# Performance work log

Measured on AMD Instinct MI355X. Metric: run time of the kernel, lower is better.

The kernel has to match this reference:

```python
import jax, jax.numpy as jnp
import numpy as np

MINUS = -100.0
PIECE_NUM = 3

def setup_inputs() -> dict:
    key = jax.random.key(0)
    kx, km = jax.random.split(key)
    B, C, L = 256, 768, 256
    x = jax.random.normal(kx, (B, C, L), dtype=jnp.float32)
    # piece ids in 0..piece_num (0 = padding -> zero row of identity embedding)
    mask = jax.random.randint(km, (B, L), 0, PIECE_NUM + 1, dtype=jnp.int64)
    return {"x": x, "mask": mask}

def reference(x, mask):
    # x: (B, C, L); mask: (B, L) ints in [0, piece_num]
    B, C, L = x.shape
    # mask_embedding weight = [zeros(1,P); I(P)], so emb(mask)[b,l,p] = (mask[b,l] == p+1)
    onehot = (mask[:, :, None] == jnp.arange(1, PIECE_NUM + 1)).astype(x.dtype)  # (B, L, P)
    # mask_embedded = 1 - emb(mask).transpose(1,2).unsqueeze(2): (B, P, 1, L)
    bias = MINUS * (1.0 - onehot.transpose(0, 2, 1))[:, :, None, :]  # (B, P, 1, L)
    # x.unsqueeze(1) + minus * mask_embedded -> (B, P, C, L); max-pool over L
    pooled = jnp.max(x[:, None, :, :] + bias, axis=-1)  # (B, P, C)
    return pooled.reshape(B, PIECE_NUM * C)  # piece-major, matches view([B, -1])
```

## Files before the change

### kernel.cpp

```cpp
#include <hip/hip_runtime.h>


constexpr int BB = 256;
constexpr int CC = 768;
constexpr int LL = 256;
constexpr int PP = 3;
constexpr float MINUS = -100.0f;

constexpr int ROWS_PER_WAVE  = 12;
constexpr int WAVES_PER_BLOCK = 4;
constexpr int ROWS_PER_BLOCK = ROWS_PER_WAVE * WAVES_PER_BLOCK;
constexpr int BLOCKS_PER_B   = CC / ROWS_PER_BLOCK;

__global__ __launch_bounds__(256) void piece_max_pool_kernel(
    const float* __restrict__ x,
    const int*   __restrict__ mask,
    float*       __restrict__ out)
{
    const int tid  = threadIdx.x;
    const int lane = tid & 63;
    const int wave = tid >> 6;
    const int blk  = blockIdx.x;
    const int b    = blk / BLOCKS_PER_B;
    const int cbase = (blk % BLOCKS_PER_B) * ROWS_PER_BLOCK + wave * ROWS_PER_WAVE;

    const int4 m4 = *reinterpret_cast<const int4*>(mask + b * LL + lane * 4);
    const int mm[4] = {m4.x, m4.y, m4.z, m4.w};
    float bias[PP][4];
#pragma unroll
    for (int p = 0; p < PP; ++p)
#pragma unroll
        for (int j = 0; j < 4; ++j)
            bias[p][j] = (mm[j] == p + 1) ? 0.0f : MINUS;

    const float* xbase = x + ((size_t)b * CC + cbase) * LL + lane * 4;

#pragma unroll
    for (int r = 0; r < ROWS_PER_WAVE; ++r) {
        const float4 v = *reinterpret_cast<const float4*>(xbase + (size_t)r * LL);
        const float vv[4] = {v.x, v.y, v.z, v.w};

        float mx[PP];
#pragma unroll
        for (int p = 0; p < PP; ++p) {
            const float m0 = fmaxf(vv[0] + bias[p][0], vv[1] + bias[p][1]);
            const float m1 = fmaxf(vv[2] + bias[p][2], vv[3] + bias[p][3]);
            mx[p] = fmaxf(m0, m1);
        }

#pragma unroll
        for (int off = 32; off >= 1; off >>= 1) {
#pragma unroll
            for (int p = 0; p < PP; ++p)
                mx[p] = fmaxf(mx[p], __shfl_xor(mx[p], off, 64));
        }

        if (lane == 0) {
            const int c = cbase + r;
            float* o = out + (size_t)b * (PP * CC) + c;
#pragma unroll
            for (int p = 0; p < PP; ++p)
                o[(size_t)p * CC] = mx[p];
        }
    }
}

extern "C" void kernel_launch(void* const* d_in, const int* in_sizes, int n_in,
                              void* d_out, int out_size, void* d_ws, size_t ws_size,
                              hipStream_t stream)
{
    const float* x    = (const float*)d_in[0];
    const int*   mask = (const int*)d_in[1];
    float*       out  = (float*)d_out;

    const int grid = BB * BLOCKS_PER_B;
    piece_max_pool_kernel<<<grid, WAVES_PER_BLOCK * 64, 0, stream>>>(x, mask, out);
}
```

Before: 278.5 us.

## Split each wave into 16-lane groups per row with nontemporal loads

```diff
diff --git a/kernel.cpp b/kernel.cpp
--- a/kernel.cpp
+++ b/kernel.cpp
@@ -7,10 +7,12 @@
 constexpr int PP = 3;
 constexpr float MINUS = -100.0f;
 
-constexpr int ROWS_PER_WAVE  = 12;
+typedef float f32x4 __attribute__((ext_vector_type(4)));
+
+constexpr int QUADS_PER_WAVE  = 3;
 constexpr int WAVES_PER_BLOCK = 4;
-constexpr int ROWS_PER_BLOCK = ROWS_PER_WAVE * WAVES_PER_BLOCK;
-constexpr int BLOCKS_PER_B   = CC / ROWS_PER_BLOCK;
+constexpr int ROWS_PER_BLOCK  = 4 * QUADS_PER_WAVE * WAVES_PER_BLOCK;
+constexpr int BLOCKS_PER_B    = CC / ROWS_PER_BLOCK;
 
 __global__ __launch_bounds__(256) void piece_max_pool_kernel(
     const float* __restrict__ x,
@@ -19,44 +21,53 @@
 {
     const int tid  = threadIdx.x;
     const int lane = tid & 63;
+    const int g    = lane & 15;
+    const int rsub = lane >> 4;
     const int wave = tid >> 6;
     const int blk  = blockIdx.x;
     const int b    = blk / BLOCKS_PER_B;
-    const int cbase = (blk % BLOCKS_PER_B) * ROWS_PER_BLOCK + wave * ROWS_PER_WAVE;
+    const int cbase = (blk % BLOCKS_PER_B) * ROWS_PER_BLOCK + wave * (4 * QUADS_PER_WAVE);
 
-    const int4 m4 = *reinterpret_cast<const int4*>(mask + b * LL + lane * 4);
-    const int mm[4] = {m4.x, m4.y, m4.z, m4.w};
-    float bias[PP][4];
+    float bias[PP][16];
 #pragma unroll
-    for (int p = 0; p < PP; ++p)
+    for (int j = 0; j < 4; ++j) {
+        const int4 m4 = *reinterpret_cast<const int4*>(mask + b * LL + j * 64 + g * 4);
+        const int mm[4] = {m4.x, m4.y, m4.z, m4.w};
 #pragma unroll
-        for (int j = 0; j < 4; ++j)
-            bias[p][j] = (mm[j] == p + 1) ? 0.0f : MINUS;
-
-    const float* xbase = x + ((size_t)b * CC + cbase) * LL + lane * 4;
+        for (int p = 0; p < PP; ++p)
+#pragma unroll
+            for (int k = 0; k < 4; ++k)
+                bias[p][j * 4 + k] = (mm[k] == p + 1) ? 0.0f : MINUS;
+    }
 
 #pragma unroll
-    for (int r = 0; r < ROWS_PER_WAVE; ++r) {
-        const float4 v = *reinterpret_cast<const float4*>(xbase + (size_t)r * LL);
-        const float vv[4] = {v.x, v.y, v.z, v.w};
+    for (int q = 0; q < QUADS_PER_WAVE; ++q) {
+        const int c = cbase + q * 4 + rsub;
+        const float* rp = x + ((size_t)b * CC + c) * LL + g * 4;
 
-        float mx[PP];
+        float mx[PP] = {-INFINITY, -INFINITY, -INFINITY};
 #pragma unroll
-        for (int p = 0; p < PP; ++p) {
-            const float m0 = fmaxf(vv[0] + bias[p][0], vv[1] + bias[p][1]);
-            const float m1 = fmaxf(vv[2] + bias[p][2], vv[3] + bias[p][3]);
-            mx[p] = fmaxf(m0, m1);
+        for (int j = 0; j < 4; ++j) {
+            const f32x4 v = __builtin_nontemporal_load(
+                reinterpret_cast<const f32x4*>(rp + j * 64));
+            const float vv[4] = {v.x, v.y, v.z, v.w};
+#pragma unroll
+            for (int p = 0; p < PP; ++p) {
+                const float m0 = fmaxf(vv[0] + bias[p][j * 4 + 0],
+                                       vv[1] + bias[p][j * 4 + 1]);
+                const float m1 = fmaxf(vv[2] + bias[p][j * 4 + 2],
+                                       vv[3] + bias[p][j * 4 + 3]);
+                mx[p] = fmaxf(mx[p], fmaxf(m0, m1));
+            }
         }
 
 #pragma unroll
-        for (int off = 32; off >= 1; off >>= 1) {
+        for (int off = 8; off >= 1; off >>= 1)
 #pragma unroll
             for (int p = 0; p < PP; ++p)
-                mx[p] = fmaxf(mx[p], __shfl_xor(mx[p], off, 64));
-        }
+                mx[p] = fmaxf(mx[p], __shfl_xor(mx[p], off, 16));
 
-        if (lane == 0) {
-            const int c = cbase + r;
+        if (g == 0) {
             float* o = out + (size_t)b * (PP * CC) + c;
 #pragma unroll
             for (int p = 0; p < PP; ++p)
```

New measurement: 253.4 us. 1.1x faster.
